# Kernel tuning notes

Hardware: AMD Instinct MI355X
Metric: run time of the kernel (lower is better)

## Reference

```python
import jax, jax.numpy as jnp
import numpy as np

HIDDEN = 2048
INTER = 1408
NUM_EXPERTS = 8
TOP_K = 2


def setup_inputs() -> dict:
    key = jax.random.key(0)
    k_x, k_rw, k_gu, k_dn = jax.random.split(key, 4)
    x = jax.random.normal(k_x, (2, 2048, HIDDEN), dtype=jnp.float32)
    router_weight = jax.random.normal(k_rw, (NUM_EXPERTS, HIDDEN), dtype=jnp.float32)
    gate_up_proj = jax.random.normal(k_gu, (NUM_EXPERTS, 2 * INTER, HIDDEN), dtype=jnp.float32) * 0.02
    down_proj = jax.random.normal(k_dn, (NUM_EXPERTS, HIDDEN, INTER), dtype=jnp.float32) * 0.02
    return {"x": x, "router_weight": router_weight, "gate_up_proj": gate_up_proj, "down_proj": down_proj}


def reference(x, router_weight, gate_up_proj, down_proj):
    E = router_weight.shape[0]
    xf = x.reshape(-1, x.shape[-1])  # [T, D]
    # Router: logits -> float32 softmax -> top-k -> renormalize
    logits = jnp.einsum('td,ed->te', xf, router_weight)
    scores = jax.nn.softmax(logits.astype(jnp.float32), axis=-1)
    topv, topi = jax.lax.top_k(scores, TOP_K)          # [T, K]
    topv = topv / jnp.sum(topv, axis=-1, keepdims=True)
    topv = topv.astype(logits.dtype)
    # Combine weights per (token, expert): zero for unselected experts,
    # so dense per-expert compute below reproduces the sparse dispatch math.
    comb = jnp.einsum('tk,tke->te', topv, jax.nn.one_hot(topi, E, dtype=topv.dtype))  # [T, E]
    # Per-expert SwiGLU FFN, dense over experts
    gu = jnp.einsum('td,efd->etf', xf, gate_up_proj)    # [E, T, 2*inter]
    gate, up = jnp.split(gu, 2, axis=-1)
    h = jax.nn.silu(gate) * up                          # [E, T, inter]
    eo = jnp.einsum('eti,edi->etd', h, down_proj)       # [E, T, D]
    out = jnp.einsum('etd,te->td', eo, comb)            # [T, D]
    return out
```

## Files before the change

kernel.cpp:

```cpp
#include <hip/hip_runtime.h>
#include <hip/hip_bf16.h>
#include <stdint.h>

#define HIDDEN 2048
#define INTER  1408
#define NE     8
#define NTOK   4096

typedef __attribute__((ext_vector_type(8))) short short8;
typedef __attribute__((ext_vector_type(4))) float f32x4;

typedef const __attribute__((address_space(1))) unsigned char* gp1_t;
typedef __attribute__((address_space(3))) unsigned char* lp3_t;

__device__ __forceinline__ void lds_cp16(const void* g, void* l) {
    __builtin_amdgcn_global_load_lds((gp1_t)g, (lp3_t)l, 16, 0, 0);
}

__device__ __forceinline__ short8 ldswz(const __hip_bfloat16 (*S)[64], int r, int col) {
    return *(const short8*)&S[r][(((col >> 3) ^ (r & 7)) << 3)];
}

__global__ void cvt_kernel(const float* __restrict__ src, __hip_bfloat16* __restrict__ dst, int n) {
    int i = (blockIdx.x * blockDim.x + threadIdx.x) * 4;
    if (i >= n) return;
    float4 v = *(const float4*)(src + i);
    __hip_bfloat162 a = __float22bfloat162_rn(make_float2(v.x, v.y));
    __hip_bfloat162 b = __float22bfloat162_rn(make_float2(v.z, v.w));
    *(__hip_bfloat162*)(dst + i)     = a;
    *(__hip_bfloat162*)(dst + i + 2) = b;
}

__global__ void router_kernel(const float* __restrict__ x, const float* __restrict__ rw,
                              int* __restrict__ counts, int* __restrict__ topk_e,
                              float* __restrict__ topk_w) {
    int wave = threadIdx.x >> 6;
    int lane = threadIdx.x & 63;
    int t = blockIdx.x * 4 + wave;
    const float* xr = x + (size_t)t * HIDDEN;
    float acc[NE] = {0.f,0.f,0.f,0.f,0.f,0.f,0.f,0.f};
    for (int i = lane; i < HIDDEN; i += 64) {
        float xi = xr[i];
        #pragma unroll
        for (int e = 0; e < NE; ++e) acc[e] += xi * rw[e * HIDDEN + i];
    }
    #pragma unroll
    for (int e = 0; e < NE; ++e) {
        #pragma unroll
        for (int off = 32; off > 0; off >>= 1) acc[e] += __shfl_xor(acc[e], off, 64);
    }
    if (lane == 0) {
        int i1 = 0; float v1 = acc[0];
        for (int e = 1; e < NE; ++e) if (acc[e] > v1) { v1 = acc[e]; i1 = e; }
        int i2 = -1; float v2 = -3.0e38f;
        for (int e = 0; e < NE; ++e) if (e != i1 && acc[e] > v2) { v2 = acc[e]; i2 = e; }
        float w1 = 1.f / (1.f + expf(v2 - v1));
        float w2 = 1.f - w1;
        topk_e[t * 2 + 0] = i1; topk_e[t * 2 + 1] = i2;
        topk_w[t * 2 + 0] = w1; topk_w[t * 2 + 1] = w2;
        atomicAdd(&counts[i1], 1);
        atomicAdd(&counts[i2], 1);
    }
}

__global__ void scan_kernel(const int* __restrict__ counts, int* __restrict__ offsets,
                            int* __restrict__ cursor) {
    if (threadIdx.x == 0) {
        int s = 0;
        for (int e = 0; e < NE; ++e) { offsets[e] = s; cursor[e] = s; s += counts[e]; }
    }
}

__global__ void scatter_kernel(const int* __restrict__ topk_e, const float* __restrict__ topk_w,
                               int* __restrict__ cursor, int* __restrict__ slot_tid,
                               float* __restrict__ slot_w) {
    int k = blockIdx.x * blockDim.x + threadIdx.x;
    if (k >= NTOK * 2) return;
    int e = topk_e[k];
    int slot = atomicAdd(&cursor[e], 1);
    slot_tid[slot] = k >> 1;
    slot_w[slot]   = topk_w[k];
}

__global__ __launch_bounds__(256) void gemm1_kernel(
    const __hip_bfloat16* __restrict__ xb,
    const __hip_bfloat16* __restrict__ gub,
    const int* __restrict__ counts, const int* __restrict__ offsets,
    const int* __restrict__ slot_tid, const float* __restrict__ slot_w,
    __hip_bfloat16* __restrict__ h)
{
    const int e  = blockIdx.z;
    const int mt = blockIdx.y;
    const int nt = blockIdx.x;
    const int count = counts[e];
    if (mt * 128 >= count) return;
    const int off = offsets[e];

    __shared__ __hip_bfloat16 As[128][64];
    __shared__ __hip_bfloat16 Bs[128][64];

    const int tid  = threadIdx.x;
    const int wave = tid >> 6;
    const int lane = tid & 63;

    const __hip_bfloat16* asrc[4];
    const __hip_bfloat16* bsrc[4];
    #pragma unroll
    for (int j = 0; j < 4; ++j) {
        int fs  = j * 256 + tid;
        int row = fs >> 3;
        int c8  = (fs & 7) ^ (row & 7);
        int rg  = mt * 128 + row;
        int rc  = rg < count ? rg : count - 1;
        int tok = slot_tid[off + rc];
        asrc[j] = xb + (size_t)tok * HIDDEN + c8 * 8;
        int grow = (row < 64) ? (nt * 64 + row) : (INTER + nt * 64 + (row - 64));
        bsrc[j] = gub + ((size_t)e * 2 * INTER + grow) * HIDDEN + c8 * 8;
    }

    f32x4 acc[2][8];
    #pragma unroll
    for (int mi = 0; mi < 2; ++mi)
        #pragma unroll
        for (int ni = 0; ni < 8; ++ni) acc[mi][ni] = (f32x4)0.f;

    const int fr = lane & 15;
    const int fk = (lane >> 4) * 8;

    for (int k0 = 0; k0 < HIDDEN; k0 += 64) {
        #pragma unroll
        for (int j = 0; j < 4; ++j) {
            lds_cp16(asrc[j] + k0, (__hip_bfloat16*)As + (j * 256 + tid) * 8);
            lds_cp16(bsrc[j] + k0, (__hip_bfloat16*)Bs + (j * 256 + tid) * 8);
        }
        __syncthreads();
        #pragma unroll
        for (int kk = 0; kk < 64; kk += 32) {
            short8 a0 = ldswz(As, wave * 32 +      fr, kk + fk);
            short8 a1 = ldswz(As, wave * 32 + 16 + fr, kk + fk);
            #pragma unroll
            for (int ni = 0; ni < 8; ++ni) {
                short8 b = ldswz(Bs, ni * 16 + fr, kk + fk);
                acc[0][ni] = __builtin_amdgcn_mfma_f32_16x16x32_bf16(a0, b, acc[0][ni], 0, 0, 0);
                acc[1][ni] = __builtin_amdgcn_mfma_f32_16x16x32_bf16(a1, b, acc[1][ni], 0, 0, 0);
            }
        }
        __syncthreads();
    }

    #pragma unroll
    for (int mi = 0; mi < 2; ++mi) {
        #pragma unroll
        for (int r = 0; r < 4; ++r) {
            int row = wave * 32 + mi * 16 + (lane >> 4) * 4 + r;
            int rg  = mt * 128 + row;
            if (rg < count) {
                float wgt = slot_w[off + rg];
                size_t base = (size_t)(off + rg) * INTER + nt * 64;
                #pragma unroll
                for (int ni = 0; ni < 4; ++ni) {
                    float g = acc[mi][ni][r];
                    float u = acc[mi][ni + 4][r];
                    float hv = g / (1.f + __expf(-g)) * u * wgt;
                    h[base + ni * 16 + fr] = __float2bfloat16(hv);
                }
            }
        }
    }
}

__global__ __launch_bounds__(256) void gemm2_kernel(
    const __hip_bfloat16* __restrict__ h,
    const __hip_bfloat16* __restrict__ dnb,
    const int* __restrict__ counts, const int* __restrict__ offsets,
    const int* __restrict__ slot_tid,
    float* __restrict__ out)
{
    const int e  = blockIdx.z;
    const int mt = blockIdx.y;
    const int nt = blockIdx.x;
    const int count = counts[e];
    if (mt * 128 >= count) return;
    const int off = offsets[e];

    __shared__ __hip_bfloat16 As[128][64];
    __shared__ __hip_bfloat16 Bs[128][64];

    const int tid  = threadIdx.x;
    const int wave = tid >> 6;
    const int lane = tid & 63;

    const __hip_bfloat16* asrc[4];
    const __hip_bfloat16* bsrc[4];
    #pragma unroll
    for (int j = 0; j < 4; ++j) {
        int fs  = j * 256 + tid;
        int row = fs >> 3;
        int c8  = (fs & 7) ^ (row & 7);
        asrc[j] = h + (size_t)(off + mt * 128 + row) * INTER + c8 * 8;
        bsrc[j] = dnb + ((size_t)e * HIDDEN + nt * 128 + row) * INTER + c8 * 8;
    }

    f32x4 acc[2][8];
    #pragma unroll
    for (int mi = 0; mi < 2; ++mi)
        #pragma unroll
        for (int ni = 0; ni < 8; ++ni) acc[mi][ni] = (f32x4)0.f;

    const int fr = lane & 15;
    const int fk = (lane >> 4) * 8;

    for (int k0 = 0; k0 < INTER; k0 += 64) {
        #pragma unroll
        for (int j = 0; j < 4; ++j) {
            lds_cp16(asrc[j] + k0, (__hip_bfloat16*)As + (j * 256 + tid) * 8);
            lds_cp16(bsrc[j] + k0, (__hip_bfloat16*)Bs + (j * 256 + tid) * 8);
        }
        __syncthreads();
        #pragma unroll
        for (int kk = 0; kk < 64; kk += 32) {
            short8 a0 = ldswz(As, wave * 32 +      fr, kk + fk);
            short8 a1 = ldswz(As, wave * 32 + 16 + fr, kk + fk);
            #pragma unroll
            for (int ni = 0; ni < 8; ++ni) {
                short8 b = ldswz(Bs, ni * 16 + fr, kk + fk);
                acc[0][ni] = __builtin_amdgcn_mfma_f32_16x16x32_bf16(a0, b, acc[0][ni], 0, 0, 0);
                acc[1][ni] = __builtin_amdgcn_mfma_f32_16x16x32_bf16(a1, b, acc[1][ni], 0, 0, 0);
            }
        }
        __syncthreads();
    }

    #pragma unroll
    for (int mi = 0; mi < 2; ++mi) {
        #pragma unroll
        for (int r = 0; r < 4; ++r) {
            int row = wave * 32 + mi * 16 + (lane >> 4) * 4 + r;
            int rg  = mt * 128 + row;
            if (rg < count) {
                int t = slot_tid[off + rg];
                float* orow = out + (size_t)t * HIDDEN + nt * 128;
                #pragma unroll
                for (int ni = 0; ni < 8; ++ni) {
                    atomicAdd(orow + ni * 16 + fr, acc[mi][ni][r]);
                }
            }
        }
    }
}

extern "C" void kernel_launch(void* const* d_in, const int* in_sizes, int n_in,
                              void* d_out, int out_size, void* d_ws, size_t ws_size,
                              hipStream_t stream)
{
    (void)in_sizes; (void)n_in; (void)ws_size;
    const float* x  = (const float*)d_in[0];
    const float* rw = (const float*)d_in[1];
    const float* gu = (const float*)d_in[2];
    const float* dn = (const float*)d_in[3];

    char* p = (char*)d_ws;
    auto take = [&](size_t bytes) { char* r = p; p += (bytes + 255) & ~(size_t)255; return r; };
    __hip_bfloat16* xb  = (__hip_bfloat16*)take((size_t)NTOK * HIDDEN * 2);
    __hip_bfloat16* gub = (__hip_bfloat16*)take((size_t)NE * 2 * INTER * HIDDEN * 2);
    __hip_bfloat16* dnb = (__hip_bfloat16*)take((size_t)NE * HIDDEN * INTER * 2);
    __hip_bfloat16* hbuf= (__hip_bfloat16*)take((size_t)(2 * NTOK + 128) * INTER * 2);
    int*   counts   = (int*)take(64);
    int*   offsets  = (int*)take(64);
    int*   cursor   = (int*)take(64);
    int*   topk_e   = (int*)take((size_t)NTOK * 2 * 4);
    float* topk_w   = (float*)take((size_t)NTOK * 2 * 4);
    int*   slot_tid = (int*)take((size_t)(2 * NTOK + 128) * 4);
    float* slot_w   = (float*)take((size_t)(2 * NTOK + 128) * 4);

    hipMemsetAsync(counts, 0, 64, stream);
    hipMemsetAsync(d_out, 0, (size_t)out_size * sizeof(float), stream);

    {
        int n = NTOK * HIDDEN;
        cvt_kernel<<<dim3((n / 4 + 255) / 256), 256, 0, stream>>>(x, xb, n);
    }
    {
        int n = NE * 2 * INTER * HIDDEN;
        cvt_kernel<<<dim3((n / 4 + 255) / 256), 256, 0, stream>>>(gu, gub, n);
    }
    {
        int n = NE * HIDDEN * INTER;
        cvt_kernel<<<dim3((n / 4 + 255) / 256), 256, 0, stream>>>(dn, dnb, n);
    }

    router_kernel<<<dim3(NTOK / 4), 256, 0, stream>>>(x, rw, counts, topk_e, topk_w);
    scan_kernel<<<dim3(1), 64, 0, stream>>>(counts, offsets, cursor);
    scatter_kernel<<<dim3((NTOK * 2) / 256), 256, 0, stream>>>(topk_e, topk_w, cursor, slot_tid, slot_w);

    gemm1_kernel<<<dim3(INTER / 64, NTOK / 128, NE), 256, 0, stream>>>(
        xb, gub, counts, offsets, slot_tid, slot_w, hbuf);
    gemm2_kernel<<<dim3(HIDDEN / 128, NTOK / 128, NE), 256, 0, stream>>>(
        hbuf, dnb, counts, offsets, slot_tid, (float*)d_out);
}
```

Baseline: 787.7 us.

## Compact expert tile grid, 2x2 wave tiling, bf16 expert outputs with combine pass

Merges the three fp32-to-bf16 conversion kernels into one launch. Replaces the dense expert×M-tile grid with a compacted list of live tiles built in the scan kernel, so no blocks launch only to exit. Both GEMMs now split the 128x128 tile across waves as a 2x2 grid of 64x64, which reuses A and B fragments across more MFMAs. The fp32 atomicAdd scatter into the output is replaced by bf16 per-slot expert outputs, written into the reused gate_up buffer, plus a gather-combine kernel, which also removes the output memset. The cost is an extra kernel and bf16 rounding of the expert outputs before they are summed.

```diff
diff --git a/kernel.cpp b/kernel.cpp
--- a/kernel.cpp
+++ b/kernel.cpp
@@ -6,6 +6,7 @@
 #define INTER  1408
 #define NE     8
 #define NTOK   4096
+#define MAXTILES 72
 
 typedef __attribute__((ext_vector_type(8))) short short8;
 typedef __attribute__((ext_vector_type(4))) float f32x4;
@@ -21,14 +22,26 @@
     return *(const short8*)&S[r][(((col >> 3) ^ (r & 7)) << 3)];
 }
 
-__global__ void cvt_kernel(const float* __restrict__ src, __hip_bfloat16* __restrict__ dst, int n) {
-    int i = (blockIdx.x * blockDim.x + threadIdx.x) * 4;
-    if (i >= n) return;
-    float4 v = *(const float4*)(src + i);
-    __hip_bfloat162 a = __float22bfloat162_rn(make_float2(v.x, v.y));
-    __hip_bfloat162 b = __float22bfloat162_rn(make_float2(v.z, v.w));
-    *(__hip_bfloat162*)(dst + i)     = a;
-    *(__hip_bfloat162*)(dst + i + 2) = b;
+__device__ __forceinline__ float bf2f(short s) {
+    union { float f; unsigned u; } u; u.u = ((unsigned)(unsigned short)s) << 16; return u.f;
+}
+
+#define C0 (NTOK * HIDDEN / 4)
+#define C1 (NE * 2 * INTER * HIDDEN / 4)
+#define C2 (NE * HIDDEN * INTER / 4)
+__global__ void cvt_all_kernel(const float* __restrict__ x, const float* __restrict__ gu,
+                               const float* __restrict__ dn,
+                               __hip_bfloat16* __restrict__ xb, __hip_bfloat16* __restrict__ gub,
+                               __hip_bfloat16* __restrict__ dnb) {
+    long c = (long)blockIdx.x * blockDim.x + threadIdx.x;
+    const float* s; __hip_bfloat16* d; long o;
+    if (c < C0)           { s = x;  d = xb;  o = c; }
+    else if (c < C0 + C1) { s = gu; d = gub; o = c - C0; }
+    else                  { s = dn; d = dnb; o = c - C0 - C1; }
+    o *= 4;
+    float4 v = *(const float4*)(s + o);
+    *(__hip_bfloat162*)(d + o)     = __float22bfloat162_rn(make_float2(v.x, v.y));
+    *(__hip_bfloat162*)(d + o + 2) = __float22bfloat162_rn(make_float2(v.z, v.w));
 }
 
 __global__ void router_kernel(const float* __restrict__ x, const float* __restrict__ rw,
@@ -64,36 +77,46 @@
 }
 
 __global__ void scan_kernel(const int* __restrict__ counts, int* __restrict__ offsets,
-                            int* __restrict__ cursor) {
+                            int* __restrict__ cursor, int* __restrict__ tiles,
+                            int* __restrict__ n_tiles) {
     if (threadIdx.x == 0) {
-        int s = 0;
-        for (int e = 0; e < NE; ++e) { offsets[e] = s; cursor[e] = s; s += counts[e]; }
+        int s = 0, nt = 0;
+        for (int e = 0; e < NE; ++e) {
+            offsets[e] = s; cursor[e] = s;
+            int c = counts[e]; s += c;
+            for (int mt = 0; mt * 128 < c; ++mt) tiles[nt++] = (e << 16) | mt;
+        }
+        n_tiles[0] = nt;
     }
 }
 
 __global__ void scatter_kernel(const int* __restrict__ topk_e, const float* __restrict__ topk_w,
                                int* __restrict__ cursor, int* __restrict__ slot_tid,
-                               float* __restrict__ slot_w) {
+                               float* __restrict__ slot_w, int* __restrict__ tok2slot) {
     int k = blockIdx.x * blockDim.x + threadIdx.x;
     if (k >= NTOK * 2) return;
     int e = topk_e[k];
     int slot = atomicAdd(&cursor[e], 1);
     slot_tid[slot] = k >> 1;
     slot_w[slot]   = topk_w[k];
+    tok2slot[k]    = slot;
 }
 
 __global__ __launch_bounds__(256) void gemm1_kernel(
     const __hip_bfloat16* __restrict__ xb,
     const __hip_bfloat16* __restrict__ gub,
     const int* __restrict__ counts, const int* __restrict__ offsets,
+    const int* __restrict__ tiles, const int* __restrict__ n_tiles,
     const int* __restrict__ slot_tid, const float* __restrict__ slot_w,
     __hip_bfloat16* __restrict__ h)
 {
-    const int e  = blockIdx.z;
-    const int mt = blockIdx.y;
+    const int ti = blockIdx.y;
+    if (ti >= n_tiles[0]) return;
+    const int tile = tiles[ti];
+    const int e  = tile >> 16;
+    const int mt = tile & 0xffff;
     const int nt = blockIdx.x;
     const int count = counts[e];
-    if (mt * 128 >= count) return;
     const int off = offsets[e];
 
     __shared__ __hip_bfloat16 As[128][64];
@@ -102,6 +125,7 @@
     const int tid  = threadIdx.x;
     const int wave = tid >> 6;
     const int lane = tid & 63;
+    const int wm = wave >> 1, wn = wave & 1;
 
     const __hip_bfloat16* asrc[4];
     const __hip_bfloat16* bsrc[4];
@@ -114,15 +138,17 @@
         int rc  = rg < count ? rg : count - 1;
         int tok = slot_tid[off + rc];
         asrc[j] = xb + (size_t)tok * HIDDEN + c8 * 8;
-        int grow = (row < 64) ? (nt * 64 + row) : (INTER + nt * 64 + (row - 64));
+        int within = row & 63, sel = within >> 5, idx = within & 31;
+        int hc  = nt * 64 + (row >> 6) * 32 + idx;
+        int grow = sel ? (INTER + hc) : hc;
         bsrc[j] = gub + ((size_t)e * 2 * INTER + grow) * HIDDEN + c8 * 8;
     }
 
-    f32x4 acc[2][8];
-    #pragma unroll
-    for (int mi = 0; mi < 2; ++mi)
-        #pragma unroll
-        for (int ni = 0; ni < 8; ++ni) acc[mi][ni] = (f32x4)0.f;
+    f32x4 acc[4][4];
+    #pragma unroll
+    for (int mi = 0; mi < 4; ++mi)
+        #pragma unroll
+        for (int ni = 0; ni < 4; ++ni) acc[mi][ni] = (f32x4)0.f;
 
     const int fr = lane & 15;
     const int fk = (lane >> 4) * 8;
@@ -136,31 +162,33 @@
         __syncthreads();
         #pragma unroll
         for (int kk = 0; kk < 64; kk += 32) {
-            short8 a0 = ldswz(As, wave * 32 +      fr, kk + fk);
-            short8 a1 = ldswz(As, wave * 32 + 16 + fr, kk + fk);
-            #pragma unroll
-            for (int ni = 0; ni < 8; ++ni) {
-                short8 b = ldswz(Bs, ni * 16 + fr, kk + fk);
-                acc[0][ni] = __builtin_amdgcn_mfma_f32_16x16x32_bf16(a0, b, acc[0][ni], 0, 0, 0);
-                acc[1][ni] = __builtin_amdgcn_mfma_f32_16x16x32_bf16(a1, b, acc[1][ni], 0, 0, 0);
-            }
+            short8 a[4], b[4];
+            #pragma unroll
+            for (int mi = 0; mi < 4; ++mi) a[mi] = ldswz(As, wm * 64 + mi * 16 + fr, kk + fk);
+            #pragma unroll
+            for (int ni = 0; ni < 4; ++ni) b[ni] = ldswz(Bs, wn * 64 + ni * 16 + fr, kk + fk);
+            #pragma unroll
+            for (int mi = 0; mi < 4; ++mi)
+                #pragma unroll
+                for (int ni = 0; ni < 4; ++ni)
+                    acc[mi][ni] = __builtin_amdgcn_mfma_f32_16x16x32_bf16(a[mi], b[ni], acc[mi][ni], 0, 0, 0);
         }
         __syncthreads();
     }
 
     #pragma unroll
-    for (int mi = 0; mi < 2; ++mi) {
+    for (int mi = 0; mi < 4; ++mi) {
         #pragma unroll
         for (int r = 0; r < 4; ++r) {
-            int row = wave * 32 + mi * 16 + (lane >> 4) * 4 + r;
+            int row = wm * 64 + mi * 16 + (lane >> 4) * 4 + r;
             int rg  = mt * 128 + row;
             if (rg < count) {
                 float wgt = slot_w[off + rg];
-                size_t base = (size_t)(off + rg) * INTER + nt * 64;
+                size_t base = (size_t)(off + rg) * INTER + nt * 64 + wn * 32;
                 #pragma unroll
-                for (int ni = 0; ni < 4; ++ni) {
+                for (int ni = 0; ni < 2; ++ni) {
                     float g = acc[mi][ni][r];
-                    float u = acc[mi][ni + 4][r];
+                    float u = acc[mi][ni + 2][r];
                     float hv = g / (1.f + __expf(-g)) * u * wgt;
                     h[base + ni * 16 + fr] = __float2bfloat16(hv);
                 }
@@ -173,14 +201,16 @@
     const __hip_bfloat16* __restrict__ h,
     const __hip_bfloat16* __restrict__ dnb,
     const int* __restrict__ counts, const int* __restrict__ offsets,
-    const int* __restrict__ slot_tid,
-    float* __restrict__ out)
+    const int* __restrict__ tiles, const int* __restrict__ n_tiles,
+    __hip_bfloat16* __restrict__ eo)
 {
-    const int e  = blockIdx.z;
-    const int mt = blockIdx.y;
+    const int ti = blockIdx.y;
+    if (ti >= n_tiles[0]) return;
+    const int tile = tiles[ti];
+    const int e  = tile >> 16;
+    const int mt = tile & 0xffff;
     const int nt = blockIdx.x;
     const int count = counts[e];
-    if (mt * 128 >= count) return;
     const int off = offsets[e];
 
     __shared__ __hip_bfloat16 As[128][64];
@@ -189,6 +219,7 @@
     const int tid  = threadIdx.x;
     const int wave = tid >> 6;
     const int lane = tid & 63;
+    const int wm = wave >> 1, wn = wave & 1;
 
     const __hip_bfloat16* asrc[4];
     const __hip_bfloat16* bsrc[4];
@@ -201,11 +232,11 @@
         bsrc[j] = dnb + ((size_t)e * HIDDEN + nt * 128 + row) * INTER + c8 * 8;
     }
 
-    f32x4 acc[2][8];
-    #pragma unroll
-    for (int mi = 0; mi < 2; ++mi)
-        #pragma unroll
-        for (int ni = 0; ni < 8; ++ni) acc[mi][ni] = (f32x4)0.f;
+    f32x4 acc[4][4];
+    #pragma unroll
+    for (int mi = 0; mi < 4; ++mi)
+        #pragma unroll
+        for (int ni = 0; ni < 4; ++ni) acc[mi][ni] = (f32x4)0.f;
 
     const int fr = lane & 15;
     const int fk = (lane >> 4) * 8;
@@ -219,41 +250,60 @@
         __syncthreads();
         #pragma unroll
         for (int kk = 0; kk < 64; kk += 32) {
-            short8 a0 = ldswz(As, wave * 32 +      fr, kk + fk);
-            short8 a1 = ldswz(As, wave * 32 + 16 + fr, kk + fk);
-            #pragma unroll
-            for (int ni = 0; ni < 8; ++ni) {
-                short8 b = ldswz(Bs, ni * 16 + fr, kk + fk);
-                acc[0][ni] = __builtin_amdgcn_mfma_f32_16x16x32_bf16(a0, b, acc[0][ni], 0, 0, 0);
-                acc[1][ni] = __builtin_amdgcn_mfma_f32_16x16x32_bf16(a1, b, acc[1][ni], 0, 0, 0);
-            }
+            short8 a[4], b[4];
+            #pragma unroll
+            for (int mi = 0; mi < 4; ++mi) a[mi] = ldswz(As, wm * 64 + mi * 16 + fr, kk + fk);
+            #pragma unroll
+            for (int ni = 0; ni < 4; ++ni) b[ni] = ldswz(Bs, wn * 64 + ni * 16 + fr, kk + fk);
+            #pragma unroll
+            for (int mi = 0; mi < 4; ++mi)
+                #pragma unroll
+                for (int ni = 0; ni < 4; ++ni)
+                    acc[mi][ni] = __builtin_amdgcn_mfma_f32_16x16x32_bf16(a[mi], b[ni], acc[mi][ni], 0, 0, 0);
         }
         __syncthreads();
     }
 
     #pragma unroll
-    for (int mi = 0; mi < 2; ++mi) {
+    for (int mi = 0; mi < 4; ++mi) {
         #pragma unroll
         for (int r = 0; r < 4; ++r) {
-            int row = wave * 32 + mi * 16 + (lane >> 4) * 4 + r;
+            int row = wm * 64 + mi * 16 + (lane >> 4) * 4 + r;
             int rg  = mt * 128 + row;
             if (rg < count) {
-                int t = slot_tid[off + rg];
-                float* orow = out + (size_t)t * HIDDEN + nt * 128;
+                size_t base = (size_t)(off + rg) * HIDDEN + nt * 128 + wn * 64;
                 #pragma unroll
-                for (int ni = 0; ni < 8; ++ni) {
-                    atomicAdd(orow + ni * 16 + fr, acc[mi][ni][r]);
-                }
+                for (int ni = 0; ni < 4; ++ni)
+                    eo[base + ni * 16 + fr] = __float2bfloat16(acc[mi][ni][r]);
             }
         }
     }
+}
+
+__global__ void combine_kernel(const __hip_bfloat16* __restrict__ eo,
+                               const int* __restrict__ tok2slot,
+                               float* __restrict__ out) {
+    int idx = blockIdx.x * blockDim.x + threadIdx.x;
+    int t = idx >> 8;
+    int c = (idx & 255) * 8;
+    int s1 = tok2slot[t * 2], s2 = tok2slot[t * 2 + 1];
+    short8 v1 = *(const short8*)(eo + (size_t)s1 * HIDDEN + c);
+    short8 v2 = *(const short8*)(eo + (size_t)s2 * HIDDEN + c);
+    float4 o0, o1;
+    o0.x = bf2f(v1[0]) + bf2f(v2[0]); o0.y = bf2f(v1[1]) + bf2f(v2[1]);
+    o0.z = bf2f(v1[2]) + bf2f(v2[2]); o0.w = bf2f(v1[3]) + bf2f(v2[3]);
+    o1.x = bf2f(v1[4]) + bf2f(v2[4]); o1.y = bf2f(v1[5]) + bf2f(v2[5]);
+    o1.z = bf2f(v1[6]) + bf2f(v2[6]); o1.w = bf2f(v1[7]) + bf2f(v2[7]);
+    float* op = out + (size_t)t * HIDDEN + c;
+    *(float4*)op = o0;
+    *(float4*)(op + 4) = o1;
 }
 
 extern "C" void kernel_launch(void* const* d_in, const int* in_sizes, int n_in,
                               void* d_out, int out_size, void* d_ws, size_t ws_size,
                               hipStream_t stream)
 {
-    (void)in_sizes; (void)n_in; (void)ws_size;
+    (void)in_sizes; (void)n_in; (void)ws_size; (void)out_size;
     const float* x  = (const float*)d_in[0];
     const float* rw = (const float*)d_in[1];
     const float* gu = (const float*)d_in[2];
@@ -268,33 +318,28 @@
     int*   counts   = (int*)take(64);
     int*   offsets  = (int*)take(64);
     int*   cursor   = (int*)take(64);
+    int*   ntile    = (int*)take(64);
+    int*   tiles    = (int*)take(MAXTILES * 4);
     int*   topk_e   = (int*)take((size_t)NTOK * 2 * 4);
     float* topk_w   = (float*)take((size_t)NTOK * 2 * 4);
     int*   slot_tid = (int*)take((size_t)(2 * NTOK + 128) * 4);
     float* slot_w   = (float*)take((size_t)(2 * NTOK + 128) * 4);
+    int*   tok2slot = (int*)take((size_t)NTOK * 2 * 4);
+    __hip_bfloat16* eo = gub;
 
     hipMemsetAsync(counts, 0, 64, stream);
-    hipMemsetAsync(d_out, 0, (size_t)out_size * sizeof(float), stream);
-
-    {
-        int n = NTOK * HIDDEN;
-        cvt_kernel<<<dim3((n / 4 + 255) / 256), 256, 0, stream>>>(x, xb, n);
-    }
-    {
-        int n = NE * 2 * INTER * HIDDEN;
-        cvt_kernel<<<dim3((n / 4 + 255) / 256), 256, 0, stream>>>(gu, gub, n);
-    }
-    {
-        int n = NE * HIDDEN * INTER;
-        cvt_kernel<<<dim3((n / 4 + 255) / 256), 256, 0, stream>>>(dn, dnb, n);
-    }
+
+    cvt_all_kernel<<<dim3((C0 + C1 + C2) / 256), 256, 0, stream>>>(x, gu, dn, xb, gub, dnb);
 
     router_kernel<<<dim3(NTOK / 4), 256, 0, stream>>>(x, rw, counts, topk_e, topk_w);
-    scan_kernel<<<dim3(1), 64, 0, stream>>>(counts, offsets, cursor);
-    scatter_kernel<<<dim3((NTOK * 2) / 256), 256, 0, stream>>>(topk_e, topk_w, cursor, slot_tid, slot_w);
-
-    gemm1_kernel<<<dim3(INTER / 64, NTOK / 128, NE), 256, 0, stream>>>(
-        xb, gub, counts, offsets, slot_tid, slot_w, hbuf);
-    gemm2_kernel<<<dim3(HIDDEN / 128, NTOK / 128, NE), 256, 0, stream>>>(
-        hbuf, dnb, counts, offsets, slot_tid, (float*)d_out);
-}
+    scan_kernel<<<dim3(1), 64, 0, stream>>>(counts, offsets, cursor, tiles, ntile);
+    scatter_kernel<<<dim3((NTOK * 2) / 256), 256, 0, stream>>>(topk_e, topk_w, cursor,
+                                                               slot_tid, slot_w, tok2slot);
+
+    gemm1_kernel<<<dim3(INTER / 64, MAXTILES), 256, 0, stream>>>(
+        xb, gub, counts, offsets, tiles, ntile, slot_tid, slot_w, hbuf);
+    gemm2_kernel<<<dim3(HIDDEN / 128, MAXTILES), 256, 0, stream>>>(
+        hbuf, dnb, counts, offsets, tiles, ntile, eo);
+    combine_kernel<<<dim3(NTOK * HIDDEN / 8 / 256), 256, 0, stream>>>(
+        eo, tok2slot, (float*)d_out);
+}
```

Result: faster. 730.3 us (-7.3%).
